# Kernel optimization log

Measured on AMD Instinct MI355X. Metric: run time of the kernel, lower is better.

The kernel has to match this reference:

```python
import jax, jax.numpy as jnp
import numpy as np

K = 5            # adaptive kernel size
C = 256          # inplanes
M = 4
CM = C // M      # 64 bottleneck channels
PLANES = 256


def _depthwise_per_sample(f, w, b, dilation, pad):
    # f: [N, Cm, H, W]; w: [N, Cm, kh, kw] per-sample depthwise weights; b: [Cm]
    # Fold batch into the channel/group dim so one grouped conv does all samples.
    N, Cm, H, W = f.shape
    x = f.reshape(1, N * Cm, H, W)
    wk = w.reshape(N * Cm, 1, w.shape[2], w.shape[3])
    out = jax.lax.conv_general_dilated(
        x, wk, window_strides=(1, 1), padding=[(pad, pad), (pad, pad)],
        rhs_dilation=(dilation, dilation), feature_group_count=N * Cm,
        dimension_numbers=("NCHW", "OIHW", "NCHW"))
    return out.reshape(N, Cm, H, W) + b[None, :, None, None]


def setup_inputs() -> dict:
    key = jax.random.key(0)
    ks = jax.random.split(key, 16)
    N, H, W = 16, 96, 96
    s = 0.05
    return {
        "x": jax.random.normal(ks[0], (N, C, H, W), jnp.float32),
        "conv_w": jax.random.normal(ks[1], (CM, C)) * s,            # 1x1 conv C->Cm
        "conv_b": jax.random.normal(ks[2], (CM,)) * s,
        "conv_k_w": jax.random.normal(ks[3], ()) * s + 1.0,          # conv_k: 1x1, 1ch
        "conv_k_b": jax.random.normal(ks[4], ()) * s,
        "conv_k2_w": jax.random.normal(ks[5], ()) * s + 1.0,         # conv_k2
        "conv_k2_b": jax.random.normal(ks[6], ()) * s,
        "conv_kernel_w": jax.random.normal(ks[7], (K * K,)) * s,     # 1 -> k*k
        "conv_kernel_b": jax.random.normal(ks[8], (K * K,)) * s,
        "conv_kernel2_w": jax.random.normal(ks[9], (9,)) * s,        # 1 -> 9
        "conv_kernel2_b": jax.random.normal(ks[10], (9,)) * s,
        "fuse_w": jax.random.normal(ks[11], (PLANES // 2, CM)) * s,  # 1x1 fuse
        "fuse_b": jax.random.normal(ks[12], (PLANES // 2,)) * s,
        "adap_b": jax.random.normal(ks[13], (CM,)) * s,              # conv_adap_kernel.bias
        "atrous_b": jax.random.normal(ks[14], (CM,)) * s,            # conv3x3_atrous bias
    }


def reference(x, conv_w, conv_b, conv_k_w, conv_k_b, conv_k2_w, conv_k2_b,
              conv_kernel_w, conv_kernel_b, conv_kernel2_w, conv_kernel2_b,
              fuse_w, fuse_b, adap_b, atrous_b):
    N = x.shape[0]
    # f = relu(1x1 conv)
    f = jax.nn.relu(jnp.einsum("oc,nchw->nohw", conv_w, x) + conv_b[None, :, None, None])
    # g = relu(conv(avg_pool(x))) -> [N, Cm]
    g = jax.nn.relu(x.mean(axis=(2, 3)) @ conv_w.T + conv_b)
    # conv_kernel (1->k*k, 1x1) applied over the Cm "spatial" axis, then conv_k (scalar affine)
    # kernel[n,c,kk] = conv_k_w * (conv_kernel_w[kk]*g[n,c] + conv_kernel_b[kk]) + conv_k_b
    ker = conv_k_w * (g[:, :, None] * conv_kernel_w[None, None, :] + conv_kernel_b) + conv_k_b
    w_dyn = ker.reshape(N, CM, K, K)
    ker2 = conv_k2_w * (g[:, :, None] * conv_kernel2_w[None, None, :] + conv_kernel2_b) + conv_k2_b
    w_atr = ker2.reshape(N, CM, 3, 3)
    # per-sample dynamic depthwise convs
    out = _depthwise_per_sample(f, w_dyn, adap_b, dilation=1, pad=(K - 1) // 2)
    out_atr = _depthwise_per_sample(f, w_atr, atrous_b, dilation=2, pad=2)
    # fuse (1x1) each branch, concat on channels
    y = jnp.einsum("oc,nchw->nohw", fuse_w, out) + fuse_b[None, :, None, None]
    y_atr = jnp.einsum("oc,nchw->nohw", fuse_w, out_atr) + fuse_b[None, :, None, None]
    return jnp.concatenate([y, y_atr], axis=1)
```

## Files before the change

kernel.cpp:

```cpp
#include <hip/hip_runtime.h>
#include <stdint.h>

#define N_S   16
#define C_IN  256
#define CMID  64
#define HH    96
#define WW    96
#define HW    9216
#define PL2   128

#define CB_OFF   0
#define KW_OFF   64
#define KB_OFF   96
#define K2W_OFF  128
#define K2B_OFF  144
#define FB_OFF   160
#define AB_OFF   288
#define ATB_OFF  352
#define SC_OFF   416

typedef __attribute__((ext_vector_type(8))) short short8;
typedef __attribute__((ext_vector_type(4))) float floatx4;

__device__ __forceinline__ float ldbf(const uint16_t* p) {
    return __uint_as_float(((uint32_t)(*p)) << 16);
}
__device__ __forceinline__ uint16_t f2bf(float f) {
    uint32_t u = __float_as_uint(f);
    u = (u + 0x7fffu + ((u >> 16) & 1u)) >> 16;
    return (uint16_t)u;
}
__device__ __forceinline__ float bfsum2(uint32_t u) {
    return __uint_as_float(u << 16) + __uint_as_float(u & 0xffff0000u);
}

__global__ __launch_bounds__(256) void k_prep(
    const uint16_t* __restrict__ xq,
    const void* conv_w, const void* conv_b, const void* ckw, const void* ckb,
    const void* ck2w, const void* ck2b, const void* kernw, const void* kernb,
    const void* kern2w, const void* kern2b, const void* fuse_w, const void* fuse_b,
    const void* adap_b, const void* atrous_b,
    int* __restrict__ flags,
    uint16_t* __restrict__ cw_bf, uint16_t* __restrict__ fw_bf,
    float* __restrict__ smalls) {
    __shared__ int cnt[2];
    int t = threadIdx.x;
    if (t < 2) cnt[t] = 0;
    __syncthreads();
    int cx = 0, cw = 0;
    const uint16_t* wq = (const uint16_t*)conv_w;
    for (int k = 0; k < 64; ++k) {
        uint16_t vx = xq[k * 256 + t];
        uint16_t vw = wq[k * 256 + t];
        if (((vx >> 7) & 0xFF) >= 0xC0) cx++;
        if (((vw >> 7) & 0xFF) >= 0xC0) cw++;
    }
    atomicAdd(&cnt[0], cx);
    atomicAdd(&cnt[1], cw);
    __syncthreads();
    if (t == 0) { flags[0] = cnt[0] > 64; flags[1] = cnt[1] > 64; }
    bool f32 = cnt[1] > 64;

    for (int i = t; i < CMID * C_IN; i += 256)
        cw_bf[i] = f32 ? f2bf(((const float*)conv_w)[i]) : ((const uint16_t*)conv_w)[i];
    for (int i = t; i < PL2 * CMID; i += 256)
        fw_bf[i] = f32 ? f2bf(((const float*)fuse_w)[i]) : ((const uint16_t*)fuse_w)[i];
    if (t < 64) {
        smalls[CB_OFF + t]  = f32 ? ((const float*)conv_b)[t]   : ldbf((const uint16_t*)conv_b + t);
        smalls[AB_OFF + t]  = f32 ? ((const float*)adap_b)[t]   : ldbf((const uint16_t*)adap_b + t);
        smalls[ATB_OFF + t] = f32 ? ((const float*)atrous_b)[t] : ldbf((const uint16_t*)atrous_b + t);
    }
    if (t < 128)
        smalls[FB_OFF + t] = f32 ? ((const float*)fuse_b)[t] : ldbf((const uint16_t*)fuse_b + t);
    if (t < 25) {
        smalls[KW_OFF + t] = f32 ? ((const float*)kernw)[t] : ldbf((const uint16_t*)kernw + t);
        smalls[KB_OFF + t] = f32 ? ((const float*)kernb)[t] : ldbf((const uint16_t*)kernb + t);
    }
    if (t < 9) {
        smalls[K2W_OFF + t] = f32 ? ((const float*)kern2w)[t] : ldbf((const uint16_t*)kern2w + t);
        smalls[K2B_OFF + t] = f32 ? ((const float*)kern2b)[t] : ldbf((const uint16_t*)kern2b + t);
    }
    if (t == 0) {
        smalls[SC_OFF + 0] = f32 ? ((const float*)ckw)[0]  : ldbf((const uint16_t*)ckw);
        smalls[SC_OFF + 1] = f32 ? ((const float*)ckb)[0]  : ldbf((const uint16_t*)ckb);
        smalls[SC_OFF + 2] = f32 ? ((const float*)ck2w)[0] : ldbf((const uint16_t*)ck2w);
        smalls[SC_OFF + 3] = f32 ? ((const float*)ck2b)[0] : ldbf((const uint16_t*)ck2b);
    }
}

__global__ __launch_bounds__(256, 4) void k_conv1x1(
    const void* __restrict__ xv, const int* __restrict__ flags,
    const uint16_t* __restrict__ cw_bf, const float* __restrict__ smalls,
    uint16_t* __restrict__ fout, float* __restrict__ partials) {
    __shared__ uint16_t x_lds[128 * 72];
    int t = threadIdx.x;
    int b = blockIdx.x;
    int n = b / 72, blk = b % 72;
    int pxb = blk * 128;
    bool xf32 = flags[0] != 0;

    int lane = t & 63, wid = t >> 6;
    int l16 = lane & 15, quad = lane >> 4;
    int nb = wid * 32;
    uint32_t* xl32 = (uint32_t*)x_lds;

    floatx4 acc[4][2];
#pragma unroll
    for (int i = 0; i < 4; ++i)
#pragma unroll
        for (int j = 0; j < 2; ++j) acc[i][j] = (floatx4){0.f, 0.f, 0.f, 0.f};

    float* pbase = partials + (size_t)(n * 72 + blk) * 256;

    for (int cc = 0; cc < 4; ++cc) {
        __syncthreads();
#pragma unroll
        for (int k = 0; k < 2; ++k) {
            int task = k * 256 + t;
            int pxg = task & 15, cp = task >> 4;
            int c = cc * 64 + cp * 2;
            int px0 = pxb + pxg * 8;
            uint16_t r0[8], r1[8];
            float s0, s1;
            if (xf32) {
                const float* xb = (const float*)xv + ((size_t)n * C_IN + c) * HW + px0;
                float4 a0 = *(const float4*)xb, a1 = *(const float4*)(xb + 4);
                float4 b0 = *(const float4*)(xb + HW), b1 = *(const float4*)(xb + HW + 4);
                s0 = (a0.x + a0.y + a0.z + a0.w) + (a1.x + a1.y + a1.z + a1.w);
                s1 = (b0.x + b0.y + b0.z + b0.w) + (b1.x + b1.y + b1.z + b1.w);
                r0[0]=f2bf(a0.x); r0[1]=f2bf(a0.y); r0[2]=f2bf(a0.z); r0[3]=f2bf(a0.w);
                r0[4]=f2bf(a1.x); r0[5]=f2bf(a1.y); r0[6]=f2bf(a1.z); r0[7]=f2bf(a1.w);
                r1[0]=f2bf(b0.x); r1[1]=f2bf(b0.y); r1[2]=f2bf(b0.z); r1[3]=f2bf(b0.w);
                r1[4]=f2bf(b1.x); r1[5]=f2bf(b1.y); r1[6]=f2bf(b1.z); r1[7]=f2bf(b1.w);
            } else {
                const uint16_t* xb = (const uint16_t*)xv + ((size_t)n * C_IN + c) * HW + px0;
                uint4 v0 = *(const uint4*)xb;
                uint4 v1 = *(const uint4*)(xb + HW);
                s0 = (bfsum2(v0.x) + bfsum2(v0.y)) + (bfsum2(v0.z) + bfsum2(v0.w));
                s1 = (bfsum2(v1.x) + bfsum2(v1.y)) + (bfsum2(v1.z) + bfsum2(v1.w));
                r0[0]=(uint16_t)v0.x; r0[1]=(uint16_t)(v0.x>>16);
                r0[2]=(uint16_t)v0.y; r0[3]=(uint16_t)(v0.y>>16);
                r0[4]=(uint16_t)v0.z; r0[5]=(uint16_t)(v0.z>>16);
                r0[6]=(uint16_t)v0.w; r0[7]=(uint16_t)(v0.w>>16);
                r1[0]=(uint16_t)v1.x; r1[1]=(uint16_t)(v1.x>>16);
                r1[2]=(uint16_t)v1.y; r1[3]=(uint16_t)(v1.y>>16);
                r1[4]=(uint16_t)v1.z; r1[5]=(uint16_t)(v1.z>>16);
                r1[6]=(uint16_t)v1.w; r1[7]=(uint16_t)(v1.w>>16);
            }
#pragma unroll
            for (int j = 0; j < 8; ++j)
                xl32[(pxg * 8 + j) * 36 + cp] = (uint32_t)r0[j] | ((uint32_t)r1[j] << 16);
#pragma unroll
            for (int off = 8; off > 0; off >>= 1) {
                s0 += __shfl_xor(s0, off, 16);
                s1 += __shfl_xor(s1, off, 16);
            }
            if ((t & 15) == 0) *(float2*)(pbase + c) = make_float2(s0, s1);
        }
        __syncthreads();
#pragma unroll
        for (int ks = 0; ks < 2; ++ks) {
            int kw = cc * 64 + ks * 32 + quad * 8;
            int kx = ks * 32 + quad * 8;
            const uint16_t* wp = cw_bf + kw;
            short8 a0 = *(const short8*)(wp + (l16)      * 256);
            short8 a1 = *(const short8*)(wp + (16 + l16) * 256);
            short8 a2 = *(const short8*)(wp + (32 + l16) * 256);
            short8 a3 = *(const short8*)(wp + (48 + l16) * 256);
#pragma unroll
            for (int nt = 0; nt < 2; ++nt) {
                short8 bv = *(const short8*)(x_lds + (nb + nt * 16 + l16) * 72 + kx);
                acc[0][nt] = __builtin_amdgcn_mfma_f32_16x16x32_bf16(a0, bv, acc[0][nt], 0, 0, 0);
                acc[1][nt] = __builtin_amdgcn_mfma_f32_16x16x32_bf16(a1, bv, acc[1][nt], 0, 0, 0);
                acc[2][nt] = __builtin_amdgcn_mfma_f32_16x16x32_bf16(a2, bv, acc[2][nt], 0, 0, 0);
                acc[3][nt] = __builtin_amdgcn_mfma_f32_16x16x32_bf16(a3, bv, acc[3][nt], 0, 0, 0);
            }
        }
    }

    __syncthreads();
#pragma unroll
    for (int mt = 0; mt < 4; ++mt) {
        int o = mt * 16 + quad * 4;
        float b0 = smalls[CB_OFF + o],     b1 = smalls[CB_OFF + o + 1];
        float b2 = smalls[CB_OFF + o + 2], b3 = smalls[CB_OFF + o + 3];
#pragma unroll
        for (int nt = 0; nt < 2; ++nt) {
            int pxl = nb + nt * 16 + l16;
            float v0 = fmaxf(acc[mt][nt][0] + b0, 0.f);
            float v1 = fmaxf(acc[mt][nt][1] + b1, 0.f);
            float v2 = fmaxf(acc[mt][nt][2] + b2, 0.f);
            float v3 = fmaxf(acc[mt][nt][3] + b3, 0.f);
            uint32_t lo = (uint32_t)f2bf(v0) | ((uint32_t)f2bf(v1) << 16);
            uint32_t hi = (uint32_t)f2bf(v2) | ((uint32_t)f2bf(v3) << 16);
            *(uint2*)(x_lds + pxl * 72 + o) = make_uint2(lo, hi);
        }
    }
    __syncthreads();
#pragma unroll
    for (int k = 0; k < 4; ++k) {
        int task = k * 256 + t;
        int o8 = (task & 7) * 8, pxl = task >> 3;
        *(uint4*)(fout + ((size_t)n * HW + pxb + pxl) * 64 + o8) =
            *(const uint4*)(x_lds + pxl * 72 + o8);
    }
}

__global__ __launch_bounds__(256) void k_weights2(
    const float* __restrict__ partials, const uint16_t* __restrict__ cw_bf,
    const float* __restrict__ smalls,
    float* __restrict__ w_dyn, float* __restrict__ w_atr) {
    __shared__ float s_sums[256];
    __shared__ float s_dot[256];
    int n = blockIdx.x, t = threadIdx.x;
    const float* pp = partials + (size_t)n * 72 * 256 + t;
    float s = 0.f;
#pragma unroll 8
    for (int k = 0; k < 72; ++k) s += pp[k * 256];
    s_sums[t] = s * (1.0f / (float)HW);
    __syncthreads();
    int cm = t & 63, seg = t >> 6;
    const uint16_t* wr = cw_bf + cm * 256 + seg * 64;
    const float* sr = s_sums + seg * 64;
    float acc = 0.f;
#pragma unroll 8
    for (int c = 0; c < 64; ++c) acc = fmaf(ldbf(wr + c), sr[c], acc);
    s_dot[t] = acc;
    __syncthreads();
    if (t < 64) {
        float a = s_dot[t] + s_dot[t + 64] + s_dot[t + 128] + s_dot[t + 192]
                + smalls[CB_OFF + t];
        float gv = fmaxf(a, 0.f);
        float ckw = smalls[SC_OFF + 0], ckb = smalls[SC_OFF + 1];
        float ck2w = smalls[SC_OFF + 2], ck2b = smalls[SC_OFF + 3];
        float* o1 = w_dyn + (size_t)(n * CMID + t) * 25;
#pragma unroll
        for (int k = 0; k < 25; ++k)
            o1[k] = fmaf(ckw, fmaf(gv, smalls[KW_OFF + k], smalls[KB_OFF + k]), ckb);
        float* o2 = w_atr + (size_t)(n * CMID + t) * 9;
#pragma unroll
        for (int k = 0; k < 9; ++k)
            o2[k] = fmaf(ck2w, fmaf(gv, smalls[K2W_OFF + k], smalls[K2B_OFF + k]), ck2b);
    }
}

__global__ __launch_bounds__(256, 4) void k_dwfuse(
    const uint16_t* __restrict__ f,
    const float* __restrict__ w_dyn, const float* __restrict__ w_atr,
    const uint16_t* __restrict__ fw_bf, const float* __restrict__ smalls,
    float* __restrict__ out) {
    __shared__ uint16_t f_lds[160 * 64];
    __shared__ uint16_t d5_lds[64 * 72];
    __shared__ uint16_t dA_lds[64 * 72];

    int t = threadIdx.x;
    int b = blockIdx.x;
    int n = b / 144, tile = b % 144;
    int y0 = (tile / 6) * 4, x0 = (tile % 6) * 16;

    int c = t >> 2, q = t & 3;
    int qx = q << 2;
    float w5[25], w9[9];
    {
        const float* wp = w_dyn + (size_t)(n * CMID + c) * 25;
#pragma unroll
        for (int k = 0; k < 25; ++k) w5[k] = wp[k];
        const float* wa = w_atr + (size_t)(n * CMID + c) * 9;
#pragma unroll
        for (int k = 0; k < 9; ++k) w9[k] = wa[k];
    }

    const uint16_t* fbase = f + (size_t)n * HW * 64;
#pragma unroll
    for (int k = 0; k < 5; ++k) {
        int task = k * 256 + t;
        int row = task >> 3, c8 = (task & 7) * 8;
        int hy = row / 20, hx = row - hy * 20;
        int y = y0 - 2 + hy, xg = x0 - 2 + hx;
        uint4 v = make_uint4(0u, 0u, 0u, 0u);
        if (y >= 0 && y < HH && xg >= 0 && xg < WW)
            v = *(const uint4*)(fbase + ((size_t)y * WW + xg) * 64 + c8);
        *(uint4*)(f_lds + row * 64 + (c8 ^ ((row & 7) << 3))) = v;
    }
    __syncthreads();

    {
        float p[8][8];
#pragma unroll
        for (int r = 0; r < 8; ++r)
#pragma unroll
            for (int cl = 0; cl < 8; ++cl) {
                int row = r * 20 + qx + cl;
                p[r][cl] = ldbf(f_lds + row * 64 + (c ^ ((row & 7) << 3)));
            }

        float b5v = smalls[AB_OFF + c], bAv = smalls[ATB_OFF + c];
        float a5[4][4], aA[4][4];
#pragma unroll
        for (int i = 0; i < 4; ++i)
#pragma unroll
            for (int j = 0; j < 4; ++j) { a5[i][j] = b5v; aA[i][j] = bAv; }

#pragma unroll
        for (int i = 0; i < 5; ++i)
#pragma unroll
            for (int j = 0; j < 5; ++j) {
                float wv = w5[i * 5 + j];
#pragma unroll
                for (int oy = 0; oy < 4; ++oy)
#pragma unroll
                    for (int ox = 0; ox < 4; ++ox)
                        a5[oy][ox] = fmaf(wv, p[oy + i][ox + j], a5[oy][ox]);
            }
#pragma unroll
        for (int i = 0; i < 3; ++i)
#pragma unroll
            for (int j = 0; j < 3; ++j) {
                float wv = w9[i * 3 + j];
#pragma unroll
                for (int oy = 0; oy < 4; ++oy)
#pragma unroll
                    for (int ox = 0; ox < 4; ++ox)
                        aA[oy][ox] = fmaf(wv, p[oy + 2 * i][ox + 2 * j], aA[oy][ox]);
            }

#pragma unroll
        for (int oy = 0; oy < 4; ++oy)
#pragma unroll
            for (int ox = 0; ox < 4; ++ox) {
                int pxo = oy * 16 + qx + ox;
                d5_lds[pxo * 72 + c] = f2bf(a5[oy][ox]);
                dA_lds[pxo * 72 + c] = f2bf(aA[oy][ox]);
            }
    }
    __syncthreads();

    {
        int lane = t & 63, wid = t >> 6;
        int l16 = lane & 15, quad = lane >> 4;
        const uint16_t* dl = (wid >= 2) ? dA_lds : d5_lds;
        int oh = (wid & 1) * 64;
        int obr = (wid >= 2) ? 128 : 0;

        floatx4 acc[4][4];
#pragma unroll
        for (int i = 0; i < 4; ++i)
#pragma unroll
            for (int j = 0; j < 4; ++j) acc[i][j] = (floatx4){0.f, 0.f, 0.f, 0.f};

#pragma unroll
        for (int ks = 0; ks < 2; ++ks) {
            int kk = ks * 32 + quad * 8;
            short8 a0 = *(const short8*)(dl + (l16)      * 72 + kk);
            short8 a1 = *(const short8*)(dl + (16 + l16) * 72 + kk);
            short8 a2 = *(const short8*)(dl + (32 + l16) * 72 + kk);
            short8 a3 = *(const short8*)(dl + (48 + l16) * 72 + kk);
#pragma unroll
            for (int nt = 0; nt < 4; ++nt) {
                short8 bv = *(const short8*)(fw_bf + (size_t)(oh + nt * 16 + l16) * 64 + kk);
                acc[0][nt] = __builtin_amdgcn_mfma_f32_16x16x32_bf16(a0, bv, acc[0][nt], 0, 0, 0);
                acc[1][nt] = __builtin_amdgcn_mfma_f32_16x16x32_bf16(a1, bv, acc[1][nt], 0, 0, 0);
                acc[2][nt] = __builtin_amdgcn_mfma_f32_16x16x32_bf16(a2, bv, acc[2][nt], 0, 0, 0);
                acc[3][nt] = __builtin_amdgcn_mfma_f32_16x16x32_bf16(a3, bv, acc[3][nt], 0, 0, 0);
            }
        }
#pragma unroll
        for (int nt = 0; nt < 4; ++nt) {
            int o = oh + nt * 16 + l16;
            float bias = smalls[FB_OFF + o];
            float* obp = out + ((size_t)(n * 256 + obr + o)) * HW + x0 + quad * 4;
#pragma unroll
            for (int mt = 0; mt < 4; ++mt) {
                float4 v;
                v.x = acc[mt][nt][0] + bias;
                v.y = acc[mt][nt][1] + bias;
                v.z = acc[mt][nt][2] + bias;
                v.w = acc[mt][nt][3] + bias;
                *(float4*)(obp + (size_t)(y0 + mt) * WW) = v;
            }
        }
    }
}

extern "C" void kernel_launch(void* const* d_in, const int* in_sizes, int n_in,
                              void* d_out, int out_size, void* d_ws, size_t ws_size,
                              hipStream_t stream) {
    float* out = (float*)d_out;

    char* ws = (char*)d_ws;
    int*      flags = (int*)ws;
    uint16_t* cw_bf = (uint16_t*)(ws + 256);
    uint16_t* fw_bf = (uint16_t*)(ws + 33024);
    float*    smalls = (float*)(ws + 49408);
    float*    partials = (float*)(ws + 65536);
    float*    w_dyn = (float*)(ws + 1245184);
    float*    w_atr = (float*)(ws + 1347584);
    uint16_t* f     = (uint16_t*)(ws + 1384448);

    k_prep<<<dim3(1), dim3(256), 0, stream>>>(
        (const uint16_t*)d_in[0],
        d_in[1], d_in[2], d_in[3], d_in[4], d_in[5], d_in[6], d_in[7], d_in[8],
        d_in[9], d_in[10], d_in[11], d_in[12], d_in[13], d_in[14],
        flags, cw_bf, fw_bf, smalls);
    k_conv1x1<<<dim3(N_S * 72), dim3(256), 0, stream>>>(
        d_in[0], flags, cw_bf, smalls, f, partials);
    k_weights2<<<dim3(N_S), dim3(256), 0, stream>>>(
        partials, cw_bf, smalls, w_dyn, w_atr);
    k_dwfuse<<<dim3(N_S * 144), dim3(256), 0, stream>>>(
        f, w_dyn, w_atr, fw_bf, smalls, out);
}
```

Measured before the change: 369.6 us.

## Software-pipeline x loads in conv1x1, swizzle LDS, parallelize prep, remap dwfuse blocks

The conv1x1 channel loop is restructured so global loads for the next 64-channel chunk are issued into registers before the MFMA phase of the current chunk, overlapping memory latency with compute. This raises register pressure, and the occupancy hint drops from 4 to 3. Several other changes ride along: an XOR swizzle on the x LDS tile and a stronger swizzle in dwfuse to cut bank conflicts, the prep kernel spread over 16 blocks, a block-index remap in dwfuse that interleaves samples across blocks, removal of the occupancy hint on dwfuse, and bf16 conversion switched to the library intrinsic with packed pairs.

```diff
diff --git a/kernel.cpp b/kernel.cpp
--- a/kernel.cpp
+++ b/kernel.cpp
@@ -1,4 +1,5 @@
 #include <hip/hip_runtime.h>
+#include <hip/hip_bf16.h>
 #include <stdint.h>
 
 #define N_S   16
@@ -26,13 +27,17 @@
     return __uint_as_float(((uint32_t)(*p)) << 16);
 }
 __device__ __forceinline__ uint16_t f2bf(float f) {
-    uint32_t u = __float_as_uint(f);
-    u = (u + 0x7fffu + ((u >> 16) & 1u)) >> 16;
-    return (uint16_t)u;
+    __hip_bfloat16 h = __float2bfloat16(f);
+    return *reinterpret_cast<uint16_t*>(&h);
+}
+__device__ __forceinline__ uint32_t pkbf(float lo, float hi) {
+    return (uint32_t)f2bf(lo) | ((uint32_t)f2bf(hi) << 16);
 }
 __device__ __forceinline__ float bfsum2(uint32_t u) {
     return __uint_as_float(u << 16) + __uint_as_float(u & 0xffff0000u);
 }
+
+#define SWZ8(row) ((((row) ^ ((row) >> 3)) & 7) << 3)
 
 __global__ __launch_bounds__(256) void k_prep(
     const uint16_t* __restrict__ xq,
@@ -58,13 +63,14 @@
     atomicAdd(&cnt[0], cx);
     atomicAdd(&cnt[1], cw);
     __syncthreads();
-    if (t == 0) { flags[0] = cnt[0] > 64; flags[1] = cnt[1] > 64; }
     bool f32 = cnt[1] > 64;
-
-    for (int i = t; i < CMID * C_IN; i += 256)
+    if (blockIdx.x == 0 && t == 0) { flags[0] = cnt[0] > 64; flags[1] = f32; }
+
+    for (int i = blockIdx.x * 256 + t; i < CMID * C_IN; i += 16 * 256)
         cw_bf[i] = f32 ? f2bf(((const float*)conv_w)[i]) : ((const uint16_t*)conv_w)[i];
-    for (int i = t; i < PL2 * CMID; i += 256)
+    for (int i = blockIdx.x * 256 + t; i < PL2 * CMID; i += 16 * 256)
         fw_bf[i] = f32 ? f2bf(((const float*)fuse_w)[i]) : ((const uint16_t*)fuse_w)[i];
+    if (blockIdx.x != 0) return;
     if (t < 64) {
         smalls[CB_OFF + t]  = f32 ? ((const float*)conv_b)[t]   : ldbf((const uint16_t*)conv_b + t);
         smalls[AB_OFF + t]  = f32 ? ((const float*)adap_b)[t]   : ldbf((const uint16_t*)adap_b + t);
@@ -88,7 +94,7 @@
     }
 }
 
-__global__ __launch_bounds__(256, 4) void k_conv1x1(
+__global__ __launch_bounds__(256, 3) void k_conv1x1(
     const void* __restrict__ xv, const int* __restrict__ flags,
     const uint16_t* __restrict__ cw_bf, const float* __restrict__ smalls,
     uint16_t* __restrict__ fout, float* __restrict__ partials) {
@@ -112,44 +118,67 @@
 
     float* pbase = partials + (size_t)(n * 72 + blk) * 256;
 
-    for (int cc = 0; cc < 4; ++cc) {
-        __syncthreads();
+    uint4 st[2][4];
+
+    auto issue = [&](int cc) {
 #pragma unroll
         for (int k = 0; k < 2; ++k) {
             int task = k * 256 + t;
             int pxg = task & 15, cp = task >> 4;
             int c = cc * 64 + cp * 2;
             int px0 = pxb + pxg * 8;
-            uint16_t r0[8], r1[8];
+            if (xf32) {
+                const float* xb = (const float*)xv + ((size_t)n * C_IN + c) * HW + px0;
+                st[k][0] = *(const uint4*)xb;
+                st[k][1] = *(const uint4*)(xb + 4);
+                st[k][2] = *(const uint4*)(xb + HW);
+                st[k][3] = *(const uint4*)(xb + HW + 4);
+            } else {
+                const uint16_t* xb = (const uint16_t*)xv + ((size_t)n * C_IN + c) * HW + px0;
+                st[k][0] = *(const uint4*)xb;
+                st[k][1] = *(const uint4*)(xb + HW);
+            }
+        }
+    };
+
+    auto convwrite = [&](int cc) {
+#pragma unroll
+        for (int k = 0; k < 2; ++k) {
+            int task = k * 256 + t;
+            int pxg = task & 15, cp = task >> 4;
+            int c = cc * 64 + cp * 2;
+            uint32_t pk[8];
             float s0, s1;
             if (xf32) {
-                const float* xb = (const float*)xv + ((size_t)n * C_IN + c) * HW + px0;
-                float4 a0 = *(const float4*)xb, a1 = *(const float4*)(xb + 4);
-                float4 b0 = *(const float4*)(xb + HW), b1 = *(const float4*)(xb + HW + 4);
-                s0 = (a0.x + a0.y + a0.z + a0.w) + (a1.x + a1.y + a1.z + a1.w);
-                s1 = (b0.x + b0.y + b0.z + b0.w) + (b1.x + b1.y + b1.z + b1.w);
-                r0[0]=f2bf(a0.x); r0[1]=f2bf(a0.y); r0[2]=f2bf(a0.z); r0[3]=f2bf(a0.w);
-                r0[4]=f2bf(a1.x); r0[5]=f2bf(a1.y); r0[6]=f2bf(a1.z); r0[7]=f2bf(a1.w);
-                r1[0]=f2bf(b0.x); r1[1]=f2bf(b0.y); r1[2]=f2bf(b0.z); r1[3]=f2bf(b0.w);
-                r1[4]=f2bf(b1.x); r1[5]=f2bf(b1.y); r1[6]=f2bf(b1.z); r1[7]=f2bf(b1.w);
+                float av[8], bv[8];
+                av[0] = __uint_as_float(st[k][0].x); av[1] = __uint_as_float(st[k][0].y);
+                av[2] = __uint_as_float(st[k][0].z); av[3] = __uint_as_float(st[k][0].w);
+                av[4] = __uint_as_float(st[k][1].x); av[5] = __uint_as_float(st[k][1].y);
+                av[6] = __uint_as_float(st[k][1].z); av[7] = __uint_as_float(st[k][1].w);
+                bv[0] = __uint_as_float(st[k][2].x); bv[1] = __uint_as_float(st[k][2].y);
+                bv[2] = __uint_as_float(st[k][2].z); bv[3] = __uint_as_float(st[k][2].w);
+                bv[4] = __uint_as_float(st[k][3].x); bv[5] = __uint_as_float(st[k][3].y);
+                bv[6] = __uint_as_float(st[k][3].z); bv[7] = __uint_as_float(st[k][3].w);
+                s0 = ((av[0] + av[1]) + (av[2] + av[3])) + ((av[4] + av[5]) + (av[6] + av[7]));
+                s1 = ((bv[0] + bv[1]) + (bv[2] + bv[3])) + ((bv[4] + bv[5]) + (bv[6] + bv[7]));
+#pragma unroll
+                for (int j = 0; j < 8; ++j) pk[j] = pkbf(av[j], bv[j]);
             } else {
-                const uint16_t* xb = (const uint16_t*)xv + ((size_t)n * C_IN + c) * HW + px0;
-                uint4 v0 = *(const uint4*)xb;
-                uint4 v1 = *(const uint4*)(xb + HW);
-                s0 = (bfsum2(v0.x) + bfsum2(v0.y)) + (bfsum2(v0.z) + bfsum2(v0.w));
-                s1 = (bfsum2(v1.x) + bfsum2(v1.y)) + (bfsum2(v1.z) + bfsum2(v1.w));
-                r0[0]=(uint16_t)v0.x; r0[1]=(uint16_t)(v0.x>>16);
-                r0[2]=(uint16_t)v0.y; r0[3]=(uint16_t)(v0.y>>16);
-                r0[4]=(uint16_t)v0.z; r0[5]=(uint16_t)(v0.z>>16);
-                r0[6]=(uint16_t)v0.w; r0[7]=(uint16_t)(v0.w>>16);
-                r1[0]=(uint16_t)v1.x; r1[1]=(uint16_t)(v1.x>>16);
-                r1[2]=(uint16_t)v1.y; r1[3]=(uint16_t)(v1.y>>16);
-                r1[4]=(uint16_t)v1.z; r1[5]=(uint16_t)(v1.z>>16);
-                r1[6]=(uint16_t)v1.w; r1[7]=(uint16_t)(v1.w>>16);
-            }
+                uint32_t u0[4] = {st[k][0].x, st[k][0].y, st[k][0].z, st[k][0].w};
+                uint32_t u1[4] = {st[k][1].x, st[k][1].y, st[k][1].z, st[k][1].w};
+                s0 = (bfsum2(u0[0]) + bfsum2(u0[1])) + (bfsum2(u0[2]) + bfsum2(u0[3]));
+                s1 = (bfsum2(u1[0]) + bfsum2(u1[1])) + (bfsum2(u1[2]) + bfsum2(u1[3]));
+#pragma unroll
+                for (int j = 0; j < 8; ++j) {
+                    uint32_t lo = (u0[j >> 1] >> ((j & 1) * 16)) & 0xffffu;
+                    uint32_t hi = (u1[j >> 1] >> ((j & 1) * 16)) & 0xffffu;
+                    pk[j] = lo | (hi << 16);
+                }
+            }
+            int swz = (pxg & 7) << 2;
 #pragma unroll
             for (int j = 0; j < 8; ++j)
-                xl32[(pxg * 8 + j) * 36 + cp] = (uint32_t)r0[j] | ((uint32_t)r1[j] << 16);
+                xl32[(pxg * 8 + j) * 36 + (cp ^ swz)] = pk[j];
 #pragma unroll
             for (int off = 8; off > 0; off >>= 1) {
                 s0 += __shfl_xor(s0, off, 16);
@@ -157,11 +186,12 @@
             }
             if ((t & 15) == 0) *(float2*)(pbase + c) = make_float2(s0, s1);
         }
-        __syncthreads();
+    };
+
+    auto mfma_ph = [&](int cc) {
 #pragma unroll
         for (int ks = 0; ks < 2; ++ks) {
             int kw = cc * 64 + ks * 32 + quad * 8;
-            int kx = ks * 32 + quad * 8;
             const uint16_t* wp = cw_bf + kw;
             short8 a0 = *(const short8*)(wp + (l16)      * 256);
             short8 a1 = *(const short8*)(wp + (16 + l16) * 256);
@@ -169,14 +199,36 @@
             short8 a3 = *(const short8*)(wp + (48 + l16) * 256);
 #pragma unroll
             for (int nt = 0; nt < 2; ++nt) {
-                short8 bv = *(const short8*)(x_lds + (nb + nt * 16 + l16) * 72 + kx);
+                int px = nb + nt * 16 + l16;
+                int kdw = (ks * 16 + quad * 4) ^ (((px >> 3) & 7) << 2);
+                short8 bv = *(const short8*)(xl32 + (size_t)px * 36 + kdw);
                 acc[0][nt] = __builtin_amdgcn_mfma_f32_16x16x32_bf16(a0, bv, acc[0][nt], 0, 0, 0);
                 acc[1][nt] = __builtin_amdgcn_mfma_f32_16x16x32_bf16(a1, bv, acc[1][nt], 0, 0, 0);
                 acc[2][nt] = __builtin_amdgcn_mfma_f32_16x16x32_bf16(a2, bv, acc[2][nt], 0, 0, 0);
                 acc[3][nt] = __builtin_amdgcn_mfma_f32_16x16x32_bf16(a3, bv, acc[3][nt], 0, 0, 0);
             }
         }
-    }
+    };
+
+    issue(0);
+    convwrite(0);
+    issue(1);
+    __syncthreads();
+    mfma_ph(0);
+    __syncthreads();
+    convwrite(1);
+    issue(2);
+    __syncthreads();
+    mfma_ph(1);
+    __syncthreads();
+    convwrite(2);
+    issue(3);
+    __syncthreads();
+    mfma_ph(2);
+    __syncthreads();
+    convwrite(3);
+    __syncthreads();
+    mfma_ph(3);
 
     __syncthreads();
 #pragma unroll
@@ -191,9 +243,7 @@
             float v1 = fmaxf(acc[mt][nt][1] + b1, 0.f);
             float v2 = fmaxf(acc[mt][nt][2] + b2, 0.f);
             float v3 = fmaxf(acc[mt][nt][3] + b3, 0.f);
-            uint32_t lo = (uint32_t)f2bf(v0) | ((uint32_t)f2bf(v1) << 16);
-            uint32_t hi = (uint32_t)f2bf(v2) | ((uint32_t)f2bf(v3) << 16);
-            *(uint2*)(x_lds + pxl * 72 + o) = make_uint2(lo, hi);
+            *(uint2*)(x_lds + pxl * 72 + o) = make_uint2(pkbf(v0, v1), pkbf(v2, v3));
         }
     }
     __syncthreads();
@@ -244,7 +294,7 @@
     }
 }
 
-__global__ __launch_bounds__(256, 4) void k_dwfuse(
+__global__ __launch_bounds__(256) void k_dwfuse(
     const uint16_t* __restrict__ f,
     const float* __restrict__ w_dyn, const float* __restrict__ w_atr,
     const uint16_t* __restrict__ fw_bf, const float* __restrict__ smalls,
@@ -254,7 +304,8 @@
     __shared__ uint16_t dA_lds[64 * 72];
 
     int t = threadIdx.x;
-    int b = blockIdx.x;
+    int orig = blockIdx.x;
+    int b = (orig & 7) * 288 + (orig >> 3);
     int n = b / 144, tile = b % 144;
     int y0 = (tile / 6) * 4, x0 = (tile % 6) * 16;
 
@@ -280,7 +331,7 @@
         uint4 v = make_uint4(0u, 0u, 0u, 0u);
         if (y >= 0 && y < HH && xg >= 0 && xg < WW)
             v = *(const uint4*)(fbase + ((size_t)y * WW + xg) * 64 + c8);
-        *(uint4*)(f_lds + row * 64 + (c8 ^ ((row & 7) << 3))) = v;
+        *(uint4*)(f_lds + row * 64 + (c8 ^ SWZ8(row))) = v;
     }
     __syncthreads();
 
@@ -291,7 +342,7 @@
 #pragma unroll
             for (int cl = 0; cl < 8; ++cl) {
                 int row = r * 20 + qx + cl;
-                p[r][cl] = ldbf(f_lds + row * 64 + (c ^ ((row & 7) << 3)));
+                p[r][cl] = ldbf(f_lds + row * 64 + (c ^ SWZ8(row)));
             }
 
         float b5v = smalls[AB_OFF + c], bAv = smalls[ATB_OFF + c];
@@ -327,10 +378,14 @@
 #pragma unroll
         for (int oy = 0; oy < 4; ++oy)
 #pragma unroll
-            for (int ox = 0; ox < 4; ++ox) {
-                int pxo = oy * 16 + qx + ox;
-                d5_lds[pxo * 72 + c] = f2bf(a5[oy][ox]);
-                dA_lds[pxo * 72 + c] = f2bf(aA[oy][ox]);
+            for (int ox = 0; ox < 4; ox += 2) {
+                int px0 = oy * 16 + qx + ox;
+                uint32_t p5 = pkbf(a5[oy][ox], a5[oy][ox + 1]);
+                uint32_t pA = pkbf(aA[oy][ox], aA[oy][ox + 1]);
+                d5_lds[px0 * 72 + c]       = (uint16_t)p5;
+                d5_lds[(px0 + 1) * 72 + c] = (uint16_t)(p5 >> 16);
+                dA_lds[px0 * 72 + c]       = (uint16_t)pA;
+                dA_lds[(px0 + 1) * 72 + c] = (uint16_t)(pA >> 16);
             }
     }
     __syncthreads();
@@ -397,7 +452,7 @@
     float*    w_atr = (float*)(ws + 1347584);
     uint16_t* f     = (uint16_t*)(ws + 1384448);
 
-    k_prep<<<dim3(1), dim3(256), 0, stream>>>(
+    k_prep<<<dim3(16), dim3(256), 0, stream>>>(
         (const uint16_t*)d_in[0],
         d_in[1], d_in[2], d_in[3], d_in[4], d_in[5], d_in[6], d_in[7], d_in[8],
         d_in[9], d_in[10], d_in[11], d_in[12], d_in[13], d_in[14],
```

Measured after the change: 393.9 us. 6.6% more time.
